# Kernel optimization log

Measured on AMD Instinct MI355X. Metric: run time of the kernel, lower is better.

Reference implementation:

```python
import jax, jax.numpy as jnp
import numpy as np

EMBED = 1024
HEADS = 16
HEAD_DIM = EMBED // HEADS
B, S = 4, 2048


def setup_inputs() -> dict:
    key = jax.random.key(0)
    ks = jax.random.split(key, 12)
    scale = 1.0 / np.sqrt(EMBED)
    inp = {
        'query': jax.random.normal(ks[0], (B, S, EMBED), jnp.float32),
        'key_in': jax.random.normal(ks[1], (B, S, EMBED), jnp.float32),
        'value': jax.random.normal(ks[2], (B, S, EMBED), jnp.float32),
        'mask': jnp.tril(jnp.ones((S, S), jnp.int32))[None, None],  # causal [1,1,S,S]
        'Wq': jax.random.normal(ks[3], (EMBED, EMBED), jnp.float32) * scale,
        'bq': jnp.zeros((EMBED,), jnp.float32),
        'Wk': jax.random.normal(ks[4], (EMBED, EMBED), jnp.float32) * scale,
        'bk': jnp.zeros((EMBED,), jnp.float32),
        'Wv': jax.random.normal(ks[5], (EMBED, EMBED), jnp.float32) * scale,
        'bv': jnp.zeros((EMBED,), jnp.float32),
        'Wo': jax.random.normal(ks[6], (EMBED, EMBED), jnp.float32) * scale,
        'bo': jnp.zeros((EMBED,), jnp.float32),
    }
    return inp


def reference(query, key_in, value, mask, Wq, bq, Wk, bk, Wv, bv, Wo, bo):
    b = query.shape[0]
    # projections (torch Linear: x @ W.T + b)
    Q = query @ Wq.T + bq
    K = key_in @ Wk.T + bk
    V = value @ Wv.T + bv
    # [B, H, S, Dh]
    Q = Q.reshape(b, -1, HEADS, HEAD_DIM).transpose(0, 2, 1, 3)
    K = K.reshape(b, -1, HEADS, HEAD_DIM).transpose(0, 2, 1, 3)
    V = V.reshape(b, -1, HEADS, HEAD_DIM).transpose(0, 2, 1, 3)
    scores = jnp.einsum('bhqd,bhkd->bhqk', Q, K) / np.sqrt(HEAD_DIM)
    scores = jnp.where(mask == 0, jnp.float32(-1e20), scores)
    probs = jax.nn.softmax(scores, axis=-1)  # dropout p=0 (eval)
    attn = jnp.einsum('bhqk,bhkd->bhqd', probs, V)
    attn = attn.transpose(0, 2, 1, 3).reshape(b, -1, EMBED)
    return attn @ Wo.T + bo
```

## Files before the change

### kernel.cpp

```cpp
#include <hip/hip_runtime.h>

typedef unsigned short u16;
typedef __bf16 bf16x8 __attribute__((ext_vector_type(8)));
typedef float f32x4 __attribute__((ext_vector_type(4)));

#define EMBED   1024
#define HEADS   16
#define HEAD_DIM 64
#define BATCH   4
#define SEQ     2048
#define MROWS   (BATCH * SEQ)

__device__ __forceinline__ u16 f2bf(float f) {
  union { __bf16 h; u16 u; } c;
  c.h = (__bf16)f;
  return c.u;
}

__device__ __forceinline__ bf16x8 cvt8(const float* p) {
  const float4 a = *(const float4*)p;
  const float4 b = *(const float4*)(p + 4);
  bf16x8 r;
  r[0] = (__bf16)a.x; r[1] = (__bf16)a.y; r[2] = (__bf16)a.z; r[3] = (__bf16)a.w;
  r[4] = (__bf16)b.x; r[5] = (__bf16)b.y; r[6] = (__bf16)b.z; r[7] = (__bf16)b.w;
  return r;
}

__device__ __forceinline__ void gload16(const u16* g, u16* lds) {
  __builtin_amdgcn_global_load_lds(
      (const __attribute__((address_space(1))) void*)g,
      (__attribute__((address_space(3))) void*)lds, 16, 0, 0);
}

__global__ __launch_bounds__(256) void cvt_bf16(
    const float* __restrict__ src, u16* __restrict__ dst, int n8)
{
  const int i = blockIdx.x * 256 + threadIdx.x;
  if (i < n8) *(bf16x8*)(dst + (size_t)i * 8) = cvt8(src + (size_t)i * 8);
}

__global__ __launch_bounds__(256) void cvt_a(
    const float* k,  u16* dk,  const float* v,  u16* dv,
    const float* wq, u16* dwq, const float* wk, u16* dwk,
    const float* wv, u16* dwv, int n8t, int n8w)
{
  int i = blockIdx.x * 256 + threadIdx.x;
  if (i < n8t) { *(bf16x8*)(dk + (size_t)i * 8) = cvt8(k + (size_t)i * 8); return; }
  i -= n8t;
  if (i < n8t) { *(bf16x8*)(dv + (size_t)i * 8) = cvt8(v + (size_t)i * 8); return; }
  i -= n8t;
  if (i < n8w) { *(bf16x8*)(dwq + (size_t)i * 8) = cvt8(wq + (size_t)i * 8); return; }
  i -= n8w;
  if (i < n8w) { *(bf16x8*)(dwk + (size_t)i * 8) = cvt8(wk + (size_t)i * 8); return; }
  i -= n8w;
  if (i < n8w) { *(bf16x8*)(dwv + (size_t)i * 8) = cvt8(wv + (size_t)i * 8); }
}

__device__ __forceinline__ void swz_block(int& m0, int& n0) {
  int bid = blockIdx.y * 8 + blockIdx.x;
  bid = (bid & 7) * 64 + (bid >> 3);
  m0 = (bid >> 3) * 128;
  n0 = (bid & 7) * 128;
}

#define GT_BK  64
#define GT_NT  (EMBED / GT_BK)
#define GT_BUF (128 * GT_BK * 2)

__global__ __launch_bounds__(256, 2) void gemm10(
    const u16* __restrict__ Aa, const u16* __restrict__ Ab,
    const u16* __restrict__ Wa, const u16* __restrict__ Wb,
    const float* __restrict__ biasa, const float* __restrict__ biasb,
    void* __restrict__ Ca, void* __restrict__ Cb, int fmode)
{
  __shared__ __align__(16) u16 smem[2 * GT_BUF];

  const int z = blockIdx.z;
  const u16* A      = z ? Ab : Aa;
  const u16* Bw     = z ? Wb : Wa;
  const float* bias = z ? biasb : biasa;
  void* C = z ? Cb : Ca;
  const int mode = z ? 1 : fmode;

  const int t    = threadIdx.x;
  const int lane = t & 63;
  const int wave = t >> 6;
  const int quad = lane >> 4;
  const int lr   = lane & 15;
  const int wr   = (wave >> 1) * 64;
  const int wc   = (wave & 1) * 64;
  int m0, n0;
  swz_block(m0, n0);

  const int sr = lane >> 3;
  const int sc = ((lane & 7) ^ sr) * 8;

  auto stage = [&](int b, int tt) {
    const int kb = tt * GT_BK;
    u16* s = smem + b * GT_BUF;
#pragma unroll
    for (int c8 = 0; c8 < 4; ++c8) {
      const int g = wave * 32 + c8 * 8;
      gload16(&A [(size_t)(m0 + g + sr) * EMBED + kb + sc], s + g * GT_BK);
      gload16(&Bw[(size_t)(n0 + g + sr) * EMBED + kb + sc], s + 128 * GT_BK + g * GT_BK);
    }
  };

  auto fragA = [&](int b, int mi, int ks) -> bf16x8 {
    const int row = wr + mi * 16 + lr;
    return *(const bf16x8*)(smem + b * GT_BUF + row * GT_BK
                            + (((ks * 4 + quad) ^ (row & 7)) << 3));
  };
  auto fragB = [&](int b, int ni, int ks) -> bf16x8 {
    const int row = wc + ni * 16 + lr;
    return *(const bf16x8*)(smem + b * GT_BUF + 128 * GT_BK + row * GT_BK
                            + (((ks * 4 + quad) ^ (row & 7)) << 3));
  };

  f32x4 acc[4][4] = {};

  stage(0, 0);
  asm volatile("s_waitcnt vmcnt(0)" ::: "memory");
  __builtin_amdgcn_s_barrier();
  __builtin_amdgcn_sched_barrier(0);

#pragma unroll 1
  for (int tt = 0; tt < GT_NT; ++tt) {
    const int cb = tt & 1;
    if (tt + 1 < GT_NT) stage(cb ^ 1, tt + 1);
#pragma unroll
    for (int ks = 0; ks < 2; ++ks) {
      bf16x8 af[4], bfr[4];
#pragma unroll
      for (int i = 0; i < 4; ++i) af[i]  = fragA(cb, i, ks);
#pragma unroll
      for (int i = 0; i < 4; ++i) bfr[i] = fragB(cb, i, ks);
      __builtin_amdgcn_s_setprio(1);
#pragma unroll
      for (int mi = 0; mi < 4; ++mi)
#pragma unroll
        for (int ni = 0; ni < 4; ++ni)
          acc[mi][ni] = __builtin_amdgcn_mfma_f32_16x16x32_bf16(af[mi], bfr[ni], acc[mi][ni], 0, 0, 0);
      __builtin_amdgcn_s_setprio(0);
    }
    asm volatile("s_waitcnt vmcnt(0)" ::: "memory");
    __builtin_amdgcn_s_barrier();
    __builtin_amdgcn_sched_barrier(0);
  }

  if (mode == 1) {
    u16* Vt = (u16*)C;
#pragma unroll
    for (int mi = 0; mi < 4; ++mi)
#pragma unroll
      for (int ni = 0; ni < 4; ++ni) {
        const int col = n0 + wc + ni * 16 + lr;
        const int hh = col >> 6, dd = col & 63;
        const float bv = bias[col];
        const int row0 = m0 + wr + mi * 16 + quad * 4;
        const int bb = row0 >> 11, s0 = row0 & 2047;
        u16 pk[4];
#pragma unroll
        for (int r = 0; r < 4; ++r) pk[r] = f2bf(acc[mi][ni][r] + bv);
        *(ushort4*)&Vt[((size_t)((bb * 16 + hh) * 64 + dd)) * SEQ + s0] = *(ushort4*)pk;
      }
  } else if (mode == 2) {
    float* Cf = (float*)C;
#pragma unroll
    for (int mi = 0; mi < 4; ++mi)
#pragma unroll
      for (int ni = 0; ni < 4; ++ni) {
        const int col = n0 + wc + ni * 16 + lr;
        const float bv = bias[col];
#pragma unroll
        for (int r = 0; r < 4; ++r) {
          const int row = m0 + wr + mi * 16 + quad * 4 + r;
          Cf[(size_t)row * EMBED + col] = acc[mi][ni][r] + bv;
        }
      }
  } else {
    u16* Cu = (u16*)C;
#pragma unroll
    for (int mi = 0; mi < 4; ++mi)
#pragma unroll
      for (int ni = 0; ni < 4; ++ni) {
        const int col = n0 + wc + ni * 16 + lr;
        const float bv = bias[col];
#pragma unroll
        for (int r = 0; r < 4; ++r) {
          const int row = m0 + wr + mi * 16 + quad * 4 + r;
          Cu[(size_t)row * EMBED + col] = f2bf(acc[mi][ni][r] + bv);
        }
      }
  }
}

#define PS_OFF 0
#define KV_OFF (64 * 72)
#define TILE_SZ (64 * 64)
__global__ __launch_bounds__(256, 3) void flash7(
    const u16* __restrict__ Qp, const u16* __restrict__ Kp,
    const u16* __restrict__ Vt, u16* __restrict__ AO)
{
  __shared__ __align__(16) u16 smem[KV_OFF + 4 * TILE_SZ];
  u16 (*Ps)[72] = (u16(*)[72])(smem + PS_OFF);

  const int t    = threadIdx.x;
  const int lane = t & 63;
  const int wave = t >> 6;
  const int quad = lane >> 4;
  const int lr   = lane & 15;
  const int bh = blockIdx.x;
  const int pr = blockIdx.y;
  const int b  = bh >> 4, h = bh & 15;
  const size_t rowbase = (size_t)b * SEQ;
  const int hcol = h * HEAD_DIM;
  const int wrow = wave * 16;
  const int sr = lane >> 3;
  const int sc = ((lane & 7) ^ sr) * 8;

  auto frag = [&](int off, int row, int chunk) -> bf16x8 {
    return *(const bf16x8*)(smem + off + row * 64 + ((chunk ^ (row & 7)) << 3));
  };

  auto stageKV = [&](int bi, int j) {
    const int kb = j * 64;
    const int ko = KV_OFF + bi * TILE_SZ;
    const int vo = KV_OFF + (2 + bi) * TILE_SZ;
#pragma unroll
    for (int c8 = 0; c8 < 2; ++c8) {
      const int g = wrow + c8 * 8;
      gload16(&Kp[(rowbase + kb + g + sr) * EMBED + hcol + sc], smem + ko + g * 64);
      gload16(&Vt[((size_t)bh * 64 + g + sr) * SEQ + kb + sc],  smem + vo + g * 64);
    }
  };

  for (int half = 0; half < 2; ++half) {
    const int qi = half ? (31 - pr) : pr;
    const int q0 = qi * 64;

    const u16* qrow = &Qp[(rowbase + q0 + wrow + lr) * EMBED + hcol];
    const bf16x8 aq0 = *(const bf16x8*)(qrow + quad * 8);
    const bf16x8 aq1 = *(const bf16x8*)(qrow + 32 + quad * 8);

    stageKV(0, 0);
    __syncthreads();

    f32x4 o_acc[4] = {};
    float lsum = 0.f;

    for (int j = 0; j <= qi; ++j) {
      if (j < qi) stageKV((j + 1) & 1, j + 1);
      const int ko = KV_OFF + (j & 1) * TILE_SZ;
      const int vo = KV_OFF + (2 + (j & 1)) * TILE_SZ;

      f32x4 st[4] = {};
#pragma unroll
      for (int ks = 0; ks < 2; ++ks) {
        const bf16x8 a = ks ? aq1 : aq0;
        bf16x8 bk[4];
#pragma unroll
        for (int mi = 0; mi < 4; ++mi) bk[mi] = frag(ko, mi * 16 + lr, ks * 4 + quad);
        __builtin_amdgcn_s_setprio(1);
#pragma unroll
        for (int mi = 0; mi < 4; ++mi)
          st[mi] = __builtin_amdgcn_mfma_f32_16x16x32_bf16(bk[mi], a, st[mi], 0, 0, 0);
        __builtin_amdgcn_s_setprio(0);
      }
      const bool diag = (j == qi);
#pragma unroll
      for (int mi = 0; mi < 4; ++mi) {
        union { ushort4 v; u16 e[4]; } pk;
#pragma unroll
        for (int r = 0; r < 4; ++r) {
          float p = __expf(st[mi][r] * 0.125f);
          if (diag && (mi * 16 + quad * 4 + r > wrow + lr)) p = 0.f;
          lsum += p;
          pk.e[r] = f2bf(p);
        }
        *(ushort4*)&Ps[wrow + lr][mi * 16 + quad * 4] = pk.v;
      }
#pragma unroll
      for (int ks = 0; ks < 2; ++ks) {
        const bf16x8 ap = *(const bf16x8*)&Ps[wrow + lr][ks * 32 + quad * 8];
        bf16x8 bv[4];
#pragma unroll
        for (int nd = 0; nd < 4; ++nd) bv[nd] = frag(vo, nd * 16 + lr, ks * 4 + quad);
        __builtin_amdgcn_s_setprio(1);
#pragma unroll
        for (int nd = 0; nd < 4; ++nd)
          o_acc[nd] = __builtin_amdgcn_mfma_f32_16x16x32_bf16(ap, bv[nd], o_acc[nd], 0, 0, 0);
        __builtin_amdgcn_s_setprio(0);
      }
      __syncthreads();
    }

    lsum += __shfl_xor(lsum, 16);
    lsum += __shfl_xor(lsum, 32);
    float linv[4];
#pragma unroll
    for (int r = 0; r < 4; ++r)
      linv[r] = 1.0f / __shfl(lsum, quad * 4 + r);
#pragma unroll
    for (int nd = 0; nd < 4; ++nd)
#pragma unroll
      for (int r = 0; r < 4; ++r)
        AO[(rowbase + q0 + wrow + quad * 4 + r) * EMBED + hcol + nd * 16 + lr]
            = f2bf(o_acc[nd][r] * linv[r]);
  }
}

extern "C" void kernel_launch(void* const* d_in, const int* in_sizes, int n_in,
                              void* d_out, int out_size, void* d_ws, size_t ws_size,
                              hipStream_t stream) {
  const float* query  = (const float*)d_in[0];
  const float* key_in = (const float*)d_in[1];
  const float* value  = (const float*)d_in[2];
  const float* Wq = (const float*)d_in[4];
  const float* bq = (const float*)d_in[5];
  const float* Wk = (const float*)d_in[6];
  const float* bk = (const float*)d_in[7];
  const float* Wv = (const float*)d_in[8];
  const float* bv = (const float*)d_in[9];
  const float* Wo = (const float*)d_in[10];
  const float* bo = (const float*)d_in[11];
  float* out = (float*)d_out;

  const size_t tsz = (size_t)MROWS * EMBED;
  const size_t wsz = (size_t)EMBED * EMBED;

  u16* Kp  = (u16*)d_ws;
  u16* Vt  = Kp + tsz;
  u16* Wob = Kp;

  u16* Kbf = (u16*)d_out;
  u16* Vbf = Kbf + tsz;
  u16* Qbf = Kbf;
  u16* Qp  = Vbf;

  u16* Wqb = (u16*)d_in[3];
  u16* Wkb = Wqb + wsz;
  u16* Wvb = Wkb + wsz;
  u16* AO  = (u16*)d_in[3];

  dim3 blk(256);
  const int n8t = (int)(tsz / 8), n8w = (int)(wsz / 8);

  cvt_a<<<(2 * n8t + 3 * n8w + 255) / 256, blk, 0, stream>>>(
      key_in, Kbf, value, Vbf, Wq, Wqb, Wk, Wkb, Wv, Wvb, n8t, n8w);

  gemm10<<<dim3(8, 64, 2), blk, 0, stream>>>(
      Kbf, Vbf, Wkb, Wvb, bk, bv, (void*)Kp, (void*)Vt, 0);

  cvt_bf16<<<n8t / 256, blk, 0, stream>>>(query, Qbf, n8t);

  gemm10<<<dim3(8, 64, 1), blk, 0, stream>>>(
      Qbf, nullptr, Wqb, nullptr, bq, nullptr, (void*)Qp, nullptr, 0);

  dim3 gattn(BATCH * HEADS, 16);
  flash7<<<gattn, blk, 0, stream>>>(Qp, Kp, Vt, AO);

  cvt_bf16<<<n8w / 256, blk, 0, stream>>>(Wo, Wob, n8w);

  gemm10<<<dim3(8, 64, 1), blk, 0, stream>>>(
      AO, nullptr, Wob, nullptr, bo, nullptr, (void*)out, nullptr, 2);
}
```

Baseline: 302.1 us.

## Process two 64-row query groups per attention block to reuse staged K/V tiles

The flash attention kernel now handles 128 query rows per block as two 64-row groups that share each staged K/V tile, with the first group skipping the last tile under the causal mask. This halves K/V global loads and LDS staging per query row, and the K fragments are loaded once for both groups. In exchange the grid has half as many blocks, which lowers parallelism. It also adds more live registers and a larger shared-memory P buffer, which may hurt occupancy.

```diff
diff --git a/kernel.cpp b/kernel.cpp
--- a/kernel.cpp
+++ b/kernel.cpp
@@ -195,15 +195,14 @@
   }
 }
 
-#define PS_OFF 0
-#define KV_OFF (64 * 72)
-#define TILE_SZ (64 * 64)
-__global__ __launch_bounds__(256, 3) void flash7(
+#define F8_KV  (128 * 72)
+#define F8_TILE (64 * 64)
+__global__ __launch_bounds__(256, 3) void flash8(
     const u16* __restrict__ Qp, const u16* __restrict__ Kp,
     const u16* __restrict__ Vt, u16* __restrict__ AO)
 {
-  __shared__ __align__(16) u16 smem[KV_OFF + 4 * TILE_SZ];
-  u16 (*Ps)[72] = (u16(*)[72])(smem + PS_OFF);
+  __shared__ __align__(16) u16 smem[F8_KV + 4 * F8_TILE];
+  u16 (*Ps)[72] = (u16(*)[72])(smem);
 
   const int t    = threadIdx.x;
   const int lane = t & 63;
@@ -225,8 +224,8 @@
 
   auto stageKV = [&](int bi, int j) {
     const int kb = j * 64;
-    const int ko = KV_OFF + bi * TILE_SZ;
-    const int vo = KV_OFF + (2 + bi) * TILE_SZ;
+    const int ko = F8_KV + bi * F8_TILE;
+    const int vo = F8_KV + (2 + bi) * F8_TILE;
 #pragma unroll
     for (int c8 = 0; c8 < 2; ++c8) {
       const int g = wrow + c8 * 8;
@@ -236,77 +235,122 @@
   };
 
   for (int half = 0; half < 2; ++half) {
-    const int qi = half ? (31 - pr) : pr;
-    const int q0 = qi * 64;
-
-    const u16* qrow = &Qp[(rowbase + q0 + wrow + lr) * EMBED + hcol];
-    const bf16x8 aq0 = *(const bf16x8*)(qrow + quad * 8);
-    const bf16x8 aq1 = *(const bf16x8*)(qrow + 32 + quad * 8);
+    const int qi = half ? (15 - pr) : pr;
+    const int q0 = qi * 128;
+    const int jmax = 2 * qi + 1;
+
+    bf16x8 aq[2][2];
+#pragma unroll
+    for (int qg = 0; qg < 2; ++qg) {
+      const u16* qrow = &Qp[(rowbase + q0 + qg * 64 + wrow + lr) * EMBED + hcol];
+      aq[qg][0] = *(const bf16x8*)(qrow + quad * 8);
+      aq[qg][1] = *(const bf16x8*)(qrow + 32 + quad * 8);
+    }
 
     stageKV(0, 0);
     __syncthreads();
 
-    f32x4 o_acc[4] = {};
-    float lsum = 0.f;
-
-    for (int j = 0; j <= qi; ++j) {
-      if (j < qi) stageKV((j + 1) & 1, j + 1);
-      const int ko = KV_OFF + (j & 1) * TILE_SZ;
-      const int vo = KV_OFF + (2 + (j & 1)) * TILE_SZ;
-
-      f32x4 st[4] = {};
+    f32x4 o0[4] = {}, o1[4] = {};
+    float ls0 = 0.f, ls1 = 0.f;
+
+    for (int j = 0; j <= jmax; ++j) {
+      if (j < jmax) stageKV((j + 1) & 1, j + 1);
+      const int ko = F8_KV + (j & 1) * F8_TILE;
+      const int vo = F8_KV + (2 + (j & 1)) * F8_TILE;
+      const bool a0 = (j <= 2 * qi);
+
+      bf16x8 bk[2][4];
+#pragma unroll
+      for (int ks = 0; ks < 2; ++ks)
+#pragma unroll
+        for (int mi = 0; mi < 4; ++mi) bk[ks][mi] = frag(ko, mi * 16 + lr, ks * 4 + quad);
+
+      if (a0) {
+        f32x4 st[4] = {};
+#pragma unroll
+        for (int ks = 0; ks < 2; ++ks) {
+          __builtin_amdgcn_s_setprio(1);
+#pragma unroll
+          for (int mi = 0; mi < 4; ++mi)
+            st[mi] = __builtin_amdgcn_mfma_f32_16x16x32_bf16(bk[ks][mi], aq[0][ks], st[mi], 0, 0, 0);
+          __builtin_amdgcn_s_setprio(0);
+        }
+        const bool diag = (j == 2 * qi);
+#pragma unroll
+        for (int mi = 0; mi < 4; ++mi) {
+          union { ushort4 v; u16 e[4]; } pk;
+#pragma unroll
+          for (int r = 0; r < 4; ++r) {
+            float p = __expf(st[mi][r] * 0.125f);
+            if (diag && (mi * 16 + quad * 4 + r > wrow + lr)) p = 0.f;
+            ls0 += p;
+            pk.e[r] = f2bf(p);
+          }
+          *(ushort4*)&Ps[wrow + lr][mi * 16 + quad * 4] = pk.v;
+        }
+      }
+      {
+        f32x4 st[4] = {};
+#pragma unroll
+        for (int ks = 0; ks < 2; ++ks) {
+          __builtin_amdgcn_s_setprio(1);
+#pragma unroll
+          for (int mi = 0; mi < 4; ++mi)
+            st[mi] = __builtin_amdgcn_mfma_f32_16x16x32_bf16(bk[ks][mi], aq[1][ks], st[mi], 0, 0, 0);
+          __builtin_amdgcn_s_setprio(0);
+        }
+        const bool diag = (j == jmax);
+#pragma unroll
+        for (int mi = 0; mi < 4; ++mi) {
+          union { ushort4 v; u16 e[4]; } pk;
+#pragma unroll
+          for (int r = 0; r < 4; ++r) {
+            float p = __expf(st[mi][r] * 0.125f);
+            if (diag && (mi * 16 + quad * 4 + r > wrow + lr)) p = 0.f;
+            ls1 += p;
+            pk.e[r] = f2bf(p);
+          }
+          *(ushort4*)&Ps[64 + wrow + lr][mi * 16 + quad * 4] = pk.v;
+        }
+      }
 #pragma unroll
       for (int ks = 0; ks < 2; ++ks) {
-        const bf16x8 a = ks ? aq1 : aq0;
-        bf16x8 bk[4];
-#pragma unroll
-        for (int mi = 0; mi < 4; ++mi) bk[mi] = frag(ko, mi * 16 + lr, ks * 4 + quad);
+        bf16x8 bv[4];
+#pragma unroll
+        for (int nd = 0; nd < 4; ++nd) bv[nd] = frag(vo, nd * 16 + lr, ks * 4 + quad);
+        const bf16x8 ap1 = *(const bf16x8*)&Ps[64 + wrow + lr][ks * 32 + quad * 8];
         __builtin_amdgcn_s_setprio(1);
-#pragma unroll
-        for (int mi = 0; mi < 4; ++mi)
-          st[mi] = __builtin_amdgcn_mfma_f32_16x16x32_bf16(bk[mi], a, st[mi], 0, 0, 0);
+        if (a0) {
+          const bf16x8 ap0 = *(const bf16x8*)&Ps[wrow + lr][ks * 32 + quad * 8];
+#pragma unroll
+          for (int nd = 0; nd < 4; ++nd)
+            o0[nd] = __builtin_amdgcn_mfma_f32_16x16x32_bf16(ap0, bv[nd], o0[nd], 0, 0, 0);
+        }
+#pragma unroll
+        for (int nd = 0; nd < 4; ++nd)
+          o1[nd] = __builtin_amdgcn_mfma_f32_16x16x32_bf16(ap1, bv[nd], o1[nd], 0, 0, 0);
         __builtin_amdgcn_s_setprio(0);
       }
-      const bool diag = (j == qi);
-#pragma unroll
-      for (int mi = 0; mi < 4; ++mi) {
-        union { ushort4 v; u16 e[4]; } pk;
-#pragma unroll
-        for (int r = 0; r < 4; ++r) {
-          float p = __expf(st[mi][r] * 0.125f);
-          if (diag && (mi * 16 + quad * 4 + r > wrow + lr)) p = 0.f;
-          lsum += p;
-          pk.e[r] = f2bf(p);
-        }
-        *(ushort4*)&Ps[wrow + lr][mi * 16 + quad * 4] = pk.v;
-      }
-#pragma unroll
-      for (int ks = 0; ks < 2; ++ks) {
-        const bf16x8 ap = *(const bf16x8*)&Ps[wrow + lr][ks * 32 + quad * 8];
-        bf16x8 bv[4];
-#pragma unroll
-        for (int nd = 0; nd < 4; ++nd) bv[nd] = frag(vo, nd * 16 + lr, ks * 4 + quad);
-        __builtin_amdgcn_s_setprio(1);
-#pragma unroll
-        for (int nd = 0; nd < 4; ++nd)
-          o_acc[nd] = __builtin_amdgcn_mfma_f32_16x16x32_bf16(ap, bv[nd], o_acc[nd], 0, 0, 0);
-        __builtin_amdgcn_s_setprio(0);
-      }
       __syncthreads();
     }
 
-    lsum += __shfl_xor(lsum, 16);
-    lsum += __shfl_xor(lsum, 32);
-    float linv[4];
-#pragma unroll
-    for (int r = 0; r < 4; ++r)
-      linv[r] = 1.0f / __shfl(lsum, quad * 4 + r);
-#pragma unroll
-    for (int nd = 0; nd < 4; ++nd)
+#pragma unroll
+    for (int qg = 0; qg < 2; ++qg) {
+      float lsum = qg ? ls1 : ls0;
+      lsum += __shfl_xor(lsum, 16);
+      lsum += __shfl_xor(lsum, 32);
+      float linv[4];
 #pragma unroll
       for (int r = 0; r < 4; ++r)
-        AO[(rowbase + q0 + wrow + quad * 4 + r) * EMBED + hcol + nd * 16 + lr]
-            = f2bf(o_acc[nd][r] * linv[r]);
+        linv[r] = 1.0f / __shfl(lsum, quad * 4 + r);
+      const f32x4* oo = qg ? o1 : o0;
+#pragma unroll
+      for (int nd = 0; nd < 4; ++nd)
+#pragma unroll
+        for (int r = 0; r < 4; ++r)
+          AO[(rowbase + q0 + qg * 64 + wrow + quad * 4 + r) * EMBED + hcol + nd * 16 + lr]
+              = f2bf(oo[nd][r] * linv[r]);
+    }
   }
 }
 
@@ -357,8 +401,8 @@
   gemm10<<<dim3(8, 64, 1), blk, 0, stream>>>(
       Qbf, nullptr, Wqb, nullptr, bq, nullptr, (void*)Qp, nullptr, 0);
 
-  dim3 gattn(BATCH * HEADS, 16);
-  flash7<<<gattn, blk, 0, stream>>>(Qp, Kp, Vt, AO);
+  dim3 gattn(BATCH * HEADS, 8);
+  flash8<<<gattn, blk, 0, stream>>>(Qp, Kp, Vt, AO);
 
   cvt_bf16<<<n8w / 256, blk, 0, stream>>>(Wo, Wob, n8w);
 
```

New measurement: 308.2 us. About the same (+2.0%).
